# Optimization experiments

Hardware: AMD Instinct MI355X
Metric: run time of the kernel (lower is better)

Reference implementation:

```python
import jax, jax.numpy as jnp
import numpy as np

DT = 0.1
N_NODES = 100000
N_EDGES = 1600000
Q = 64


def setup_inputs() -> dict:
    key = jax.random.key(0)
    k1, k2, k3, k4, k5, k6, k7 = jax.random.split(key, 7)
    f = jax.random.uniform(k1, (N_NODES, Q), dtype=jnp.float32)
    collision = jax.random.normal(k2, (N_NODES, Q), dtype=jnp.float32)
    source = jax.random.normal(k3, (N_NODES, Q), dtype=jnp.float32)
    weight = jax.random.uniform(k4, (N_EDGES,), dtype=jnp.float32)
    xi = jax.random.normal(k5, (Q,), dtype=jnp.float32)
    src = jax.random.randint(k6, (N_EDGES,), 0, N_NODES)
    dst = jax.random.randint(k7, (N_EDGES,), 0, N_NODES)
    edge_index = jnp.stack([src, dst], axis=0)  # [2, E]
    return {
        "f_distribution": f,
        "collision_term": collision,
        "source_term": source,
        "edge_weight": weight,
        "xi_velocities": xi,
        "edge_index": edge_index,
    }


def reference(f_distribution, collision_term, source_term, edge_weight, xi_velocities, edge_index):
    src = edge_index[0]
    dst = edge_index[1]
    n = f_distribution.shape[0]

    # node degrees (DGL graph.out_degrees / in_degrees stored as ndata)
    ones_e = jnp.ones(src.shape[0], dtype=f_distribution.dtype)
    out_deg = jax.ops.segment_sum(ones_e, src, num_segments=n)
    in_deg = jax.ops.segment_sum(ones_e, dst, num_segments=n)
    out_deg = jnp.maximum(out_deg, 1.0)  # guard isolated nodes
    in_deg = jnp.maximum(in_deg, 1.0)

    f = jnp.clip(f_distribution, 0.0, None)

    # per-edge distribution difference f[dst] - f[src], shared by both passes
    f_diff = f[dst] - f[src]  # [E, Q]

    # inflow: message on original graph, q_ij = 1/out_degree(src), reduce at dst
    scale_in = (edge_weight / out_deg[src])[:, None] * xi_velocities[None, :]
    inflow = jax.ops.segment_sum(scale_in * f_diff, dst, num_segments=n)

    # outflow: on reversed graph: diff = f[rev_src]-f[rev_dst] = f[dst]-f[src],
    # q_ij = 1/in_degree(rev_dst) = 1/in_degree(src), reduce at rev_dst = src
    scale_out = (edge_weight / in_deg[src])[:, None] * xi_velocities[None, :]
    outflow = jax.ops.segment_sum(scale_out * f_diff, src, num_segments=n)

    transport = outflow - inflow
    f_new = f - DT * (transport - collision_term - source_term)
    return jnp.clip(f_new, 0.0, None)
```

## Files before the change

### kernel.cpp

```cpp
#include <hip/hip_runtime.h>

#define DT_CONST 0.1f
constexpr int Q = 64;
constexpr int SCAN_CHUNK = 1024;

constexpr int NPB = 128;
constexpr int CE  = 4096;
constexpr int EPC = 2 * CE;
constexpr int CAP = 4480;
constexpr int MAXCH = 512;
constexpr int P1T = 1024;

__global__ void count_kernel(const int* __restrict__ src, const int* __restrict__ dst,
                             int* __restrict__ cnt_out, int* __restrict__ cnt_in, int E) {
    int i = blockIdx.x * blockDim.x + threadIdx.x;
    int stride = gridDim.x * blockDim.x;
    for (int e = i; e < E; e += stride) {
        atomicAdd(&cnt_out[src[e]], 1);
        atomicAdd(&cnt_in[dst[e]], 1);
    }
}

__global__ __launch_bounds__(P1T, 8) void p1_kernel(
        const int* __restrict__ esrc, const int* __restrict__ edst,
        const float* __restrict__ w,
        const int* __restrict__ cnt_out, const int* __restrict__ cnt_in,
        int2* __restrict__ gstage, unsigned short* __restrict__ lofs_g,
        int E, int NB) {
    __shared__ int counts[1025];
    __shared__ int lofs[1025];
    __shared__ int work[1024];
    __shared__ alignas(16) int2 staged[EPC];

    int c = blockIdx.x;
    int e0 = c * CE;
    int ce = min(CE, E - e0);
    int tid = threadIdx.x;

    for (int i = tid; i < NB; i += P1T) counts[i] = 0;
    __syncthreads();

    int k4 = tid * 4;
    int4 se = make_int4(0, 0, 0, 0), de = make_int4(0, 0, 0, 0);
    float4 wv = make_float4(0.f, 0.f, 0.f, 0.f);
    int nmine = 0;
    if (k4 + 3 < ce) {
        se = *(const int4*)(esrc + e0 + k4);
        de = *(const int4*)(edst + e0 + k4);
        wv = *(const float4*)(w + e0 + k4);
        nmine = 4;
    } else if (k4 < ce) {
        int r = ce - k4;
        int* sp = &se.x; int* dp = &de.x; float* wp = &wv.x;
        for (int j = 0; j < r; ++j) {
            sp[j] = esrc[e0 + k4 + j];
            dp[j] = edst[e0 + k4 + j];
            wp[j] = w[e0 + k4 + j];
        }
        nmine = r;
    }
    {
        const int* sp = &se.x; const int* dp = &de.x;
        for (int j = 0; j < nmine; ++j) {
            atomicAdd(&counts[sp[j] >> 7], 1);
            atomicAdd(&counts[dp[j] >> 7], 1);
        }
    }
    __syncthreads();

    if (tid < 64) {
        int lane = tid;
        int carry = 0;
        for (int base = 0; base < NB; base += 64) {
            int idx = base + lane;
            int v = (idx < NB) ? counts[idx] : 0;
            int inc = v;
            for (int s = 1; s < 64; s <<= 1) {
                int t = __shfl_up(inc, s);
                if (lane >= s) inc += t;
            }
            if (idx < NB) lofs[idx] = carry + inc - v;
            carry += __shfl(inc, 63);
        }
        if (lane == 0) lofs[NB] = carry;
    }
    __syncthreads();

    for (int i = tid; i < NB; i += P1T) work[i] = lofs[i];
    __syncthreads();

    {
        const int* sp = &se.x; const int* dp = &de.x; const float* wp = &wv.x;
        for (int j = 0; j < nmine; ++j) {
            int s = sp[j], d = dp[j];
            float ww = wp[j];
            float w1 = ww / (float)max(cnt_in[s], 1);
            int pa = atomicAdd(&work[s >> 7], 1);
            staged[pa] = make_int2(((s & 127) << 17) | d, __float_as_int(w1));
            float w2 = ww / (float)max(cnt_out[s], 1);
            int pb = atomicAdd(&work[d >> 7], 1);
            staged[pb] = make_int2(((d & 127) << 17) | s, __float_as_int(w2));
        }
    }
    __syncthreads();

    int ne = 2 * ce;
    int4* gout4 = (int4*)(gstage + (size_t)c * EPC);
    const int4* st4 = (const int4*)staged;
    int ne2 = ne >> 1;
    for (int k = tid; k < ne2; k += P1T) gout4[k] = st4[k];
    if (ne & 1) { if (tid == 0) gstage[(size_t)c * EPC + ne - 1] = staged[ne - 1]; }
    unsigned short* lrow = lofs_g + (size_t)c * (NB + 1);
    for (int i = tid; i <= NB; i += P1T) lrow[i] = (unsigned short)lofs[i];
}

__global__ __launch_bounds__(512, 8) void pg_kernel(
        const float* __restrict__ f, const float* __restrict__ coll,
        const float* __restrict__ srct, const float* __restrict__ xi,
        const int* __restrict__ cnt_out, const int* __restrict__ cnt_in,
        const int2* __restrict__ gstage, const unsigned short* __restrict__ lofs_g,
        float* __restrict__ out, int N, int NB, int nchunks) {
    __shared__ unsigned short cum[MAXCH + 1];
    __shared__ unsigned short cstart[MAXCH];
    __shared__ int loff[NPB + 1];
    __shared__ int lcn[NPB];
    __shared__ int work[NPB];
    __shared__ alignas(16) int2 sorted[CAP];

    int b = blockIdx.x;
    int node0 = b * NPB;
    int nn = min(NPB, N - node0);
    int tid = threadIdx.x;
    int wid = tid >> 6, lane = tid & 63;

    for (int c = tid; c < nchunks; c += 512) {
        const unsigned short* lr = lofs_g + (size_t)c * (NB + 1);
        int lo = lr[b], hi = lr[b + 1];
        cstart[c] = (unsigned short)lo;
        cum[c] = (unsigned short)(hi - lo);
    }
    for (int i = tid; i < NPB; i += 512) {
        int v = node0 + i;
        lcn[i] = (i < nn) ? (cnt_out[v] + cnt_in[v]) : 0;
    }
    __syncthreads();

    if (wid == 0) {
        int carry = 0;
        for (int base = 0; base < nchunks; base += 64) {
            int idx = base + lane;
            int v = (idx < nchunks) ? (int)cum[idx] : 0;
            int inc = v;
            for (int s = 1; s < 64; s <<= 1) {
                int t = __shfl_up(inc, s);
                if (lane >= s) inc += t;
            }
            if (idx < nchunks) cum[idx] = (unsigned short)(carry + inc - v);
            carry += __shfl(inc, 63);
        }
        if (lane == 0) cum[nchunks] = (unsigned short)carry;
    }
    if (wid == 1) {
        int carry = 0;
        for (int base = 0; base < NPB; base += 64) {
            int idx = base + lane;
            int v = lcn[idx];
            int inc = v;
            for (int s = 1; s < 64; s <<= 1) {
                int t = __shfl_up(inc, s);
                if (lane >= s) inc += t;
            }
            loff[idx] = carry + inc - v;
            carry += __shfl(inc, 63);
        }
        if (lane == 0) loff[NPB] = carry;
    }
    __syncthreads();

    int tb = cum[nchunks];
    if (tb > CAP) tb = CAP;

    for (int i = tid; i < NPB; i += 512) work[i] = loff[i];
    __syncthreads();

    for (int r = tid; r < tb; r += 512) {
        int lo = 0, hi = nchunks - 1;
        while (lo < hi) {
            int mid = (lo + hi + 1) >> 1;
            if ((int)cum[mid] <= r) lo = mid; else hi = mid - 1;
        }
        int c = lo;
        int2 e = gstage[(size_t)c * EPC + (int)cstart[c] + (r - (int)cum[c])];
        int local = (e.x >> 17) & 127;
        int pos = atomicAdd(&work[local], 1);
        if (pos < CAP) sorted[pos] = make_int2(e.x & 131071, e.y);
    }
    __syncthreads();

    float xiv = xi[lane];
    for (int i = wid; i < nn; i += 8) {
        int st = loff[i], dg = lcn[i];
        float acc = 0.0f, S = 0.0f;
        int k = 0;
        for (; k + 8 <= dg; k += 8) {
            int2 e0 = sorted[st + k],     e1 = sorted[st + k + 1];
            int2 e2 = sorted[st + k + 2], e3 = sorted[st + k + 3];
            int2 e4 = sorted[st + k + 4], e5 = sorted[st + k + 5];
            int2 e6 = sorted[st + k + 6], e7 = sorted[st + k + 7];
            float f0 = f[(size_t)e0.x * Q + lane];
            float f1 = f[(size_t)e1.x * Q + lane];
            float f2 = f[(size_t)e2.x * Q + lane];
            float f3 = f[(size_t)e3.x * Q + lane];
            float f4 = f[(size_t)e4.x * Q + lane];
            float f5 = f[(size_t)e5.x * Q + lane];
            float f6 = f[(size_t)e6.x * Q + lane];
            float f7 = f[(size_t)e7.x * Q + lane];
            float w0 = __int_as_float(e0.y), w1 = __int_as_float(e1.y);
            float w2 = __int_as_float(e2.y), w3 = __int_as_float(e3.y);
            float w4 = __int_as_float(e4.y), w5 = __int_as_float(e5.y);
            float w6 = __int_as_float(e6.y), w7 = __int_as_float(e7.y);
            acc += w0 * fmaxf(f0, 0.0f); S += w0;
            acc += w1 * fmaxf(f1, 0.0f); S += w1;
            acc += w2 * fmaxf(f2, 0.0f); S += w2;
            acc += w3 * fmaxf(f3, 0.0f); S += w3;
            acc += w4 * fmaxf(f4, 0.0f); S += w4;
            acc += w5 * fmaxf(f5, 0.0f); S += w5;
            acc += w6 * fmaxf(f6, 0.0f); S += w6;
            acc += w7 * fmaxf(f7, 0.0f); S += w7;
        }
        for (; k < dg; ++k) {
            int2 e = sorted[st + k];
            float fn = f[(size_t)e.x * Q + lane];
            float wv = __int_as_float(e.y);
            acc += wv * fmaxf(fn, 0.0f); S += wv;
        }
        size_t idx = (size_t)(node0 + i) * Q + lane;
        float fv = fmaxf(f[idx], 0.0f);
        float t = xiv * (acc - fv * S);
        float r = fv - DT_CONST * (t - coll[idx] - srct[idx]);
        out[idx] = fmaxf(r, 0.0f);
    }
}

__global__ void scanA_kernel(const int* __restrict__ cnt_out, const int* __restrict__ cnt_in,
                             int* __restrict__ off_out, int* __restrict__ off_in,
                             int* __restrict__ bsum, int nblk, int n) {
    int b = blockIdx.x;
    const int* cnt; int* off; int* bs;
    if (b < nblk) { cnt = cnt_out; off = off_out; bs = bsum; }
    else          { cnt = cnt_in;  off = off_in;  bs = bsum + nblk; b -= nblk; }
    int i = b * SCAN_CHUNK + threadIdx.x;
    __shared__ int tmp[SCAN_CHUNK];
    int v = (i < n) ? cnt[i] : 0;
    tmp[threadIdx.x] = v;
    __syncthreads();
    for (int s = 1; s < SCAN_CHUNK; s <<= 1) {
        int t = (threadIdx.x >= (unsigned)s) ? tmp[threadIdx.x - s] : 0;
        __syncthreads();
        tmp[threadIdx.x] += t;
        __syncthreads();
    }
    if (i < n) off[i] = tmp[threadIdx.x] - v;
    if (threadIdx.x == SCAN_CHUNK - 1) bs[b] = tmp[SCAN_CHUNK - 1];
}

__global__ void scanB_kernel(int* __restrict__ bsum, int nblk) {
    __shared__ int tmp[SCAN_CHUNK];
    for (int dir = 0; dir < 2; ++dir) {
        int* bs = bsum + dir * nblk;
        int v = (threadIdx.x < (unsigned)nblk) ? bs[threadIdx.x] : 0;
        tmp[threadIdx.x] = v;
        __syncthreads();
        for (int s = 1; s < SCAN_CHUNK; s <<= 1) {
            int t = (threadIdx.x >= (unsigned)s) ? tmp[threadIdx.x - s] : 0;
            __syncthreads();
            tmp[threadIdx.x] += t;
            __syncthreads();
        }
        if (threadIdx.x < (unsigned)nblk) bs[threadIdx.x] = tmp[threadIdx.x] - v;
        __syncthreads();
    }
}

__global__ void scanC_kernel(int* __restrict__ off_out, int* __restrict__ off_in,
                             const int* __restrict__ bsum, int nblk, int n) {
    int b = blockIdx.x;
    bool isOut = b < nblk;
    int bb = isOut ? b : b - nblk;
    int i = bb * SCAN_CHUNK + threadIdx.x;
    if (i >= n) return;
    if (isOut) off_out[i] += bsum[b];
    else       off_in[i]  += bsum[b];
}

__global__ void fill_kernel(const int* __restrict__ src, const int* __restrict__ dst,
                            const float* __restrict__ w, const int* __restrict__ cnt_out,
                            int* __restrict__ off_out, int* __restrict__ off_in,
                            int2* __restrict__ pair_out, int2* __restrict__ pair_in, int E) {
    int i = blockIdx.x * blockDim.x + threadIdx.x;
    int stride = gridDim.x * blockDim.x;
    for (int e = i; e < E; e += stride) {
        int s = src[e], d = dst[e];
        float ww = w[e];
        int p = atomicAdd(&off_out[s], 1);
        pair_out[p] = make_int2(d, __float_as_int(ww));
        float sc = ww / (float)max(cnt_out[s], 1);
        int q = atomicAdd(&off_in[d], 1);
        pair_in[q] = make_int2(s, __float_as_int(sc));
    }
}

__global__ void gather_kernel(const float* __restrict__ f,
                              const float* __restrict__ coll,
                              const float* __restrict__ srct,
                              const float* __restrict__ xi,
                              const int* __restrict__ off_out, const int* __restrict__ cnt_out,
                              const int2* __restrict__ pair_out,
                              const int* __restrict__ off_in, const int* __restrict__ cnt_in,
                              const int2* __restrict__ pair_in,
                              float* __restrict__ out, int N) {
    int v = blockIdx.x * (blockDim.x >> 6) + (threadIdx.x >> 6);
    if (v >= N) return;
    int lane = threadIdx.x & 63;
    float fv = fmaxf(f[(size_t)v * Q + lane], 0.0f);
    float acc_out = 0.0f, acc_in = 0.0f;
    {
        int dg = cnt_out[v];
        int st = off_out[v] - dg;
        for (int base = 0; base < dg; base += 64) {
            int m = min(64, dg - base);
            int2 pr = make_int2(0, 0);
            if (lane < m) pr = pair_out[st + base + lane];
            for (int j = 0; j < m; ++j) {
                int   n2 = __shfl(pr.x, j);
                float w2 = __int_as_float(__shfl(pr.y, j));
                float fd = fmaxf(f[(size_t)n2 * Q + lane], 0.0f);
                acc_out += w2 * (fd - fv);
            }
        }
    }
    {
        int dg = cnt_in[v];
        int st = off_in[v] - dg;
        for (int base = 0; base < dg; base += 64) {
            int m = min(64, dg - base);
            int2 pr = make_int2(0, 0);
            if (lane < m) pr = pair_in[st + base + lane];
            for (int j = 0; j < m; ++j) {
                int   n2 = __shfl(pr.x, j);
                float w2 = __int_as_float(__shfl(pr.y, j));
                float fs = fmaxf(f[(size_t)n2 * Q + lane], 0.0f);
                acc_in += w2 * (fv - fs);
            }
        }
    }
    float indeg = (float)max(cnt_in[v], 1);
    float transport = xi[lane] * (acc_out / indeg - acc_in);
    size_t idx = (size_t)v * Q + lane;
    float r = fv - DT_CONST * (transport - coll[idx] - srct[idx]);
    out[idx] = fmaxf(r, 0.0f);
}

__global__ void deg_kernel(const int* __restrict__ src, const int* __restrict__ dst,
                           float* __restrict__ out_deg, float* __restrict__ in_deg, int E) {
    int i = blockIdx.x * blockDim.x + threadIdx.x;
    int stride = gridDim.x * blockDim.x;
    for (int e = i; e < E; e += stride) {
        atomicAdd(&out_deg[src[e]], 1.0f);
        atomicAdd(&in_deg[dst[e]], 1.0f);
    }
}

__global__ void scatter_kernel(const float* __restrict__ f, const float* __restrict__ w,
                               const float* __restrict__ xi, const int* __restrict__ src,
                               const int* __restrict__ dst, const float* __restrict__ out_deg,
                               const float* __restrict__ in_deg, float* __restrict__ transport,
                               int E) {
    int e = blockIdx.x * (blockDim.x >> 6) + (threadIdx.x >> 6);
    if (e >= E) return;
    int lane = threadIdx.x & 63;
    int s = src[e], d = dst[e];
    float ww = w[e];
    float s_out = ww / fmaxf(in_deg[s], 1.0f);
    float s_in  = ww / fmaxf(out_deg[s], 1.0f);
    float fs = fmaxf(f[(size_t)s * Q + lane], 0.0f);
    float fd = fmaxf(f[(size_t)d * Q + lane], 0.0f);
    float val = xi[lane] * (fd - fs);
    atomicAdd(&transport[(size_t)s * Q + lane],  s_out * val);
    atomicAdd(&transport[(size_t)d * Q + lane], -s_in  * val);
}

__global__ void final_kernel(const float* __restrict__ f, const float* __restrict__ coll,
                             const float* __restrict__ srct, float* __restrict__ out, int n4) {
    int i = blockIdx.x * blockDim.x + threadIdx.x;
    if (i >= n4) return;
    float4 t  = ((const float4*)out)[i];
    float4 fv = ((const float4*)f)[i];
    float4 c  = ((const float4*)coll)[i];
    float4 s  = ((const float4*)srct)[i];
    float4 r;
    r.x = fmaxf(fmaxf(fv.x, 0.0f) - DT_CONST * (t.x - c.x - s.x), 0.0f);
    r.y = fmaxf(fmaxf(fv.y, 0.0f) - DT_CONST * (t.y - c.y - s.y), 0.0f);
    r.z = fmaxf(fmaxf(fv.z, 0.0f) - DT_CONST * (t.z - c.z - s.z), 0.0f);
    r.w = fmaxf(fmaxf(fv.w, 0.0f) - DT_CONST * (t.w - c.w - s.w), 0.0f);
    ((float4*)out)[i] = r;
}

extern "C" void kernel_launch(void* const* d_in, const int* in_sizes, int n_in,
                              void* d_out, int out_size, void* d_ws, size_t ws_size,
                              hipStream_t stream) {
    const float* f    = (const float*)d_in[0];
    const float* coll = (const float*)d_in[1];
    const float* srct = (const float*)d_in[2];
    const float* w    = (const float*)d_in[3];
    const float* xi   = (const float*)d_in[4];
    const int*   eidx = (const int*)d_in[5];

    int N = in_sizes[0] / Q;
    int E = in_sizes[3];
    const int* esrc = eidx;
    const int* edst = eidx + E;
    float* out = (float*)d_out;

    int NB = (N + NPB - 1) / NPB;
    int nchunks = (E + CE - 1) / CE;
    size_t need1 = (size_t)nchunks * EPC * sizeof(int2)
                 + (size_t)2 * N * sizeof(int)
                 + (size_t)nchunks * (NB + 1) * sizeof(unsigned short);

    int nblk = (N + SCAN_CHUNK - 1) / SCAN_CHUNK;
    size_t need2 = ((size_t)4 * N + 2 * nblk + 256 + (size_t)4 * E) * 4;

    if (N <= 131072 && NB <= 1024 && nchunks <= MAXCH && ws_size >= need1) {
        int2* gstage = (int2*)d_ws;
        int* cnt_out = (int*)(gstage + (size_t)nchunks * EPC);
        int* cnt_in  = cnt_out + N;
        unsigned short* lofs = (unsigned short*)(cnt_in + N);

        hipMemsetAsync(cnt_out, 0, (size_t)2 * N * sizeof(int), stream);
        count_kernel<<<2048, 256, 0, stream>>>(esrc, edst, cnt_out, cnt_in, E);
        p1_kernel<<<nchunks, P1T, 0, stream>>>(esrc, edst, w, cnt_out, cnt_in,
                                               gstage, lofs, E, NB);
        pg_kernel<<<NB, 512, 0, stream>>>(f, coll, srct, xi,
                                          cnt_out, cnt_in, gstage, lofs,
                                          out, N, NB, nchunks);
    } else if (ws_size >= need2) {
        int* cnt_out = (int*)d_ws;
        int* cnt_in  = cnt_out + N;
        int* off_out = cnt_in + N;
        int* off_in  = off_out + N;
        int* bsum    = off_in + N;
        int2* pair_out = (int2*)(bsum + 2 * nblk + 256);
        int2* pair_in  = pair_out + E;

        hipMemsetAsync(cnt_out, 0, (size_t)2 * N * sizeof(int), stream);
        count_kernel<<<2048, 256, 0, stream>>>(esrc, edst, cnt_out, cnt_in, E);
        scanA_kernel<<<2 * nblk, SCAN_CHUNK, 0, stream>>>(cnt_out, cnt_in,
                                                          off_out, off_in, bsum, nblk, N);
        scanB_kernel<<<1, SCAN_CHUNK, 0, stream>>>(bsum, nblk);
        scanC_kernel<<<2 * nblk, SCAN_CHUNK, 0, stream>>>(off_out, off_in, bsum, nblk, N);
        fill_kernel<<<2048, 256, 0, stream>>>(esrc, edst, w, cnt_out,
                                              off_out, off_in, pair_out, pair_in, E);
        int gblocks = (N + 3) / 4;
        gather_kernel<<<gblocks, 256, 0, stream>>>(f, coll, srct, xi,
                                                   off_out, cnt_out, pair_out,
                                                   off_in, cnt_in, pair_in, out, N);
    } else {
        float* out_deg = (float*)d_ws;
        float* in_deg  = out_deg + N;
        hipMemsetAsync(out, 0, (size_t)N * Q * sizeof(float), stream);
        hipMemsetAsync(d_ws, 0, (size_t)2 * N * sizeof(float), stream);
        deg_kernel<<<1024, 256, 0, stream>>>(esrc, edst, out_deg, in_deg, E);
        int blocks = (E + 3) / 4;
        scatter_kernel<<<blocks, 256, 0, stream>>>(f, w, xi, esrc, edst,
                                                   out_deg, in_deg, out, E);
        int n4 = (N * Q) / 4;
        final_kernel<<<(n4 + 255) / 256, 256, 0, stream>>>(f, coll, srct, out, n4);
    }
}
```

Measured before the change: 406.6 us.

## Derive degrees from staged buckets, drop count kernel, gather neighbors in bf16

Removes the global-atomic count pass and the memset. p1 now stages raw weights plus a direction bit, and a new deg2 kernel derives packed in/out degrees per node block from the staged buckets. The gather kernel splits each node's edges into two bins: one normalised by the node's own in-degree, the other divided by the neighbour's out-degree, which is looked up per edge. p1 also converts clipped f to bf16 so the neighbour gathers read half the bytes. The cost is lower precision in the aggregated sums, an extra kernel that re-reads the staged edges, and extra random degree loads per outflow edge.

```diff
diff --git a/kernel.cpp b/kernel.cpp
--- a/kernel.cpp
+++ b/kernel.cpp
@@ -11,22 +11,20 @@
 constexpr int MAXCH = 512;
 constexpr int P1T = 1024;
 
-__global__ void count_kernel(const int* __restrict__ src, const int* __restrict__ dst,
-                             int* __restrict__ cnt_out, int* __restrict__ cnt_in, int E) {
-    int i = blockIdx.x * blockDim.x + threadIdx.x;
-    int stride = gridDim.x * blockDim.x;
-    for (int e = i; e < E; e += stride) {
-        atomicAdd(&cnt_out[src[e]], 1);
-        atomicAdd(&cnt_in[dst[e]], 1);
-    }
-}
-
+__device__ inline unsigned short f2bf_clip(float x) {
+    x = fmaxf(x, 0.0f);
+    unsigned u = __float_as_uint(x);
+    u += 0x7FFF + ((u >> 16) & 1);
+    return (unsigned short)(u >> 16);
+}
+
+template<bool CVT>
 __global__ __launch_bounds__(P1T, 8) void p1_kernel(
         const int* __restrict__ esrc, const int* __restrict__ edst,
-        const float* __restrict__ w,
-        const int* __restrict__ cnt_out, const int* __restrict__ cnt_in,
+        const float* __restrict__ w, const float* __restrict__ f,
+        unsigned short* __restrict__ fb,
         int2* __restrict__ gstage, unsigned short* __restrict__ lofs_g,
-        int E, int NB) {
+        int E, int NB, int N) {
     __shared__ int counts[1025];
     __shared__ int lofs[1025];
     __shared__ int work[1024];
@@ -36,6 +34,18 @@
     int e0 = c * CE;
     int ce = min(CE, E - e0);
     int tid = threadIdx.x;
+
+    if (CVT) {
+        size_t n4 = (size_t)N * Q / 4;
+        size_t gthreads = (size_t)gridDim.x * P1T;
+        for (size_t i = (size_t)c * P1T + tid; i < n4; i += gthreads) {
+            float4 v = ((const float4*)f)[i];
+            ushort4 o;
+            o.x = f2bf_clip(v.x); o.y = f2bf_clip(v.y);
+            o.z = f2bf_clip(v.z); o.w = f2bf_clip(v.w);
+            ((ushort4*)fb)[i] = o;
+        }
+    }
 
     for (int i = tid; i < NB; i += P1T) counts[i] = 0;
     __syncthreads();
@@ -93,13 +103,11 @@
         const int* sp = &se.x; const int* dp = &de.x; const float* wp = &wv.x;
         for (int j = 0; j < nmine; ++j) {
             int s = sp[j], d = dp[j];
-            float ww = wp[j];
-            float w1 = ww / (float)max(cnt_in[s], 1);
+            int wb = __float_as_int(wp[j]);
             int pa = atomicAdd(&work[s >> 7], 1);
-            staged[pa] = make_int2(((s & 127) << 17) | d, __float_as_int(w1));
-            float w2 = ww / (float)max(cnt_out[s], 1);
+            staged[pa] = make_int2(((s & 127) << 17) | d, wb);
             int pb = atomicAdd(&work[d >> 7], 1);
-            staged[pb] = make_int2(((d & 127) << 17) | s, __float_as_int(w2));
+            staged[pb] = make_int2(0x1000000 | ((d & 127) << 17) | s, wb);
         }
     }
     __syncthreads();
@@ -109,40 +117,31 @@
     const int4* st4 = (const int4*)staged;
     int ne2 = ne >> 1;
     for (int k = tid; k < ne2; k += P1T) gout4[k] = st4[k];
-    if (ne & 1) { if (tid == 0) gstage[(size_t)c * EPC + ne - 1] = staged[ne - 1]; }
+    if ((ne & 1) && tid == 0) gstage[(size_t)c * EPC + ne - 1] = staged[ne - 1];
     unsigned short* lrow = lofs_g + (size_t)c * (NB + 1);
     for (int i = tid; i <= NB; i += P1T) lrow[i] = (unsigned short)lofs[i];
 }
 
-__global__ __launch_bounds__(512, 8) void pg_kernel(
-        const float* __restrict__ f, const float* __restrict__ coll,
-        const float* __restrict__ srct, const float* __restrict__ xi,
-        const int* __restrict__ cnt_out, const int* __restrict__ cnt_in,
+__global__ __launch_bounds__(256) void deg2_kernel(
         const int2* __restrict__ gstage, const unsigned short* __restrict__ lofs_g,
-        float* __restrict__ out, int N, int NB, int nchunks) {
+        int* __restrict__ deg, int N, int NB, int nchunks) {
     __shared__ unsigned short cum[MAXCH + 1];
     __shared__ unsigned short cstart[MAXCH];
-    __shared__ int loff[NPB + 1];
-    __shared__ int lcn[NPB];
-    __shared__ int work[NPB];
-    __shared__ alignas(16) int2 sorted[CAP];
+    __shared__ int cnt[NPB];
 
     int b = blockIdx.x;
     int node0 = b * NPB;
     int nn = min(NPB, N - node0);
     int tid = threadIdx.x;
-    int wid = tid >> 6, lane = tid & 63;
-
-    for (int c = tid; c < nchunks; c += 512) {
+    int lane = tid & 63, wid = tid >> 6;
+
+    for (int c = tid; c < nchunks; c += 256) {
         const unsigned short* lr = lofs_g + (size_t)c * (NB + 1);
         int lo = lr[b], hi = lr[b + 1];
         cstart[c] = (unsigned short)lo;
         cum[c] = (unsigned short)(hi - lo);
     }
-    for (int i = tid; i < NPB; i += 512) {
-        int v = node0 + i;
-        lcn[i] = (i < nn) ? (cnt_out[v] + cnt_in[v]) : 0;
-    }
+    for (int i = tid; i < NPB; i += 256) cnt[i] = 0;
     __syncthreads();
 
     if (wid == 0) {
@@ -160,11 +159,76 @@
         }
         if (lane == 0) cum[nchunks] = (unsigned short)carry;
     }
+    __syncthreads();
+
+    int tb = cum[nchunks];
+    for (int r = tid; r < tb; r += 256) {
+        int lo = 0, hi = nchunks - 1;
+        while (lo < hi) {
+            int mid = (lo + hi + 1) >> 1;
+            if ((int)cum[mid] <= r) lo = mid; else hi = mid - 1;
+        }
+        int c = lo;
+        int x = gstage[(size_t)c * EPC + (int)cstart[c] + (r - (int)cum[c])].x;
+        int local = (x >> 17) & 127;
+        int t = (x >> 24) & 1;
+        atomicAdd(&cnt[local], 1 << (t * 16));
+    }
+    __syncthreads();
+    for (int i = tid; i < nn; i += 256) deg[node0 + i] = cnt[i];
+}
+
+template<bool BF16>
+__global__ __launch_bounds__(512, 8) void pg_kernel(
+        const float* __restrict__ f, const unsigned short* __restrict__ fb,
+        const float* __restrict__ coll, const float* __restrict__ srct,
+        const float* __restrict__ xi, const int* __restrict__ deg_g,
+        const int2* __restrict__ gstage, const unsigned short* __restrict__ lofs_g,
+        float* __restrict__ out, int N, int NB, int nchunks) {
+    __shared__ unsigned short cum[MAXCH + 1];
+    __shared__ unsigned short cstart[MAXCH];
+    __shared__ int loff[2 * NPB + 1];
+    __shared__ int work[2 * NPB];
+    __shared__ int degl[NPB];
+    __shared__ alignas(16) int2 sorted[CAP];
+
+    int b = blockIdx.x;
+    int node0 = b * NPB;
+    int nn = min(NPB, N - node0);
+    int tid = threadIdx.x;
+    int wid = tid >> 6, lane = tid & 63;
+
+    for (int c = tid; c < nchunks; c += 512) {
+        const unsigned short* lr = lofs_g + (size_t)c * (NB + 1);
+        int lo = lr[b], hi = lr[b + 1];
+        cstart[c] = (unsigned short)lo;
+        cum[c] = (unsigned short)(hi - lo);
+    }
+    for (int i = tid; i < NPB; i += 512)
+        degl[i] = (i < nn) ? deg_g[node0 + i] : 0;
+    __syncthreads();
+
+    if (wid == 0) {
+        int carry = 0;
+        for (int base = 0; base < nchunks; base += 64) {
+            int idx = base + lane;
+            int v = (idx < nchunks) ? (int)cum[idx] : 0;
+            int inc = v;
+            for (int s = 1; s < 64; s <<= 1) {
+                int t = __shfl_up(inc, s);
+                if (lane >= s) inc += t;
+            }
+            if (idx < nchunks) cum[idx] = (unsigned short)(carry + inc - v);
+            carry += __shfl(inc, 63);
+        }
+        if (lane == 0) cum[nchunks] = (unsigned short)carry;
+    }
     if (wid == 1) {
         int carry = 0;
-        for (int base = 0; base < NPB; base += 64) {
+        for (int base = 0; base < 2 * NPB; base += 64) {
             int idx = base + lane;
-            int v = lcn[idx];
+            int d = degl[idx >> 1];
+            int v = (idx & 1) ? (d >> 16) : (d & 0xFFFF);
             int inc = v;
             for (int s = 1; s < 64; s <<= 1) {
                 int t = __shfl_up(inc, s);
@@ -173,14 +237,14 @@
             loff[idx] = carry + inc - v;
             carry += __shfl(inc, 63);
         }
-        if (lane == 0) loff[NPB] = carry;
+        if (lane == 0) loff[2 * NPB] = carry;
     }
     __syncthreads();
 
     int tb = cum[nchunks];
     if (tb > CAP) tb = CAP;
 
-    for (int i = tid; i < NPB; i += 512) work[i] = loff[i];
+    for (int i = tid; i < 2 * NPB; i += 512) work[i] = loff[i];
     __syncthreads();
 
     for (int r = tid; r < tb; r += 512) {
@@ -192,53 +256,84 @@
         int c = lo;
         int2 e = gstage[(size_t)c * EPC + (int)cstart[c] + (r - (int)cum[c])];
         int local = (e.x >> 17) & 127;
-        int pos = atomicAdd(&work[local], 1);
-        if (pos < CAP) sorted[pos] = make_int2(e.x & 131071, e.y);
+        int bin = local * 2 + ((e.x >> 24) & 1);
+        int pos = atomicAdd(&work[bin], 1);
+        if (pos < CAP) sorted[pos] = make_int2(e.x & 0x1FFFF, e.y);
     }
     __syncthreads();
 
     float xiv = xi[lane];
     for (int i = wid; i < nn; i += 8) {
-        int st = loff[i], dg = lcn[i];
-        float acc = 0.0f, S = 0.0f;
-        int k = 0;
-        for (; k + 8 <= dg; k += 8) {
-            int2 e0 = sorted[st + k],     e1 = sorted[st + k + 1];
-            int2 e2 = sorted[st + k + 2], e3 = sorted[st + k + 3];
-            int2 e4 = sorted[st + k + 4], e5 = sorted[st + k + 5];
-            int2 e6 = sorted[st + k + 6], e7 = sorted[st + k + 7];
-            float f0 = f[(size_t)e0.x * Q + lane];
-            float f1 = f[(size_t)e1.x * Q + lane];
-            float f2 = f[(size_t)e2.x * Q + lane];
-            float f3 = f[(size_t)e3.x * Q + lane];
-            float f4 = f[(size_t)e4.x * Q + lane];
-            float f5 = f[(size_t)e5.x * Q + lane];
-            float f6 = f[(size_t)e6.x * Q + lane];
-            float f7 = f[(size_t)e7.x * Q + lane];
+        int dl = degl[i];
+        float rin = __fdividef(1.0f, (float)max(dl >> 16, 1));
+        int stA = min(loff[2 * i], CAP);
+        int mid = min(loff[2 * i + 1], CAP);
+        int end = min(loff[2 * i + 2], CAP);
+        float accA = 0.0f, SA = 0.0f, accB = 0.0f, SB = 0.0f;
+
+#define LOADF(nbr) (BF16 ? __uint_as_float((unsigned)fb[(size_t)(nbr) * Q + lane] << 16) \
+                         : fmaxf(f[(size_t)(nbr) * Q + lane], 0.0f))
+        int k = stA;
+        for (; k + 8 <= mid; k += 8) {
+            int2 e0 = sorted[k],     e1 = sorted[k + 1];
+            int2 e2 = sorted[k + 2], e3 = sorted[k + 3];
+            int2 e4 = sorted[k + 4], e5 = sorted[k + 5];
+            int2 e6 = sorted[k + 6], e7 = sorted[k + 7];
+            float f0 = LOADF(e0.x), f1 = LOADF(e1.x), f2 = LOADF(e2.x), f3 = LOADF(e3.x);
+            float f4 = LOADF(e4.x), f5 = LOADF(e5.x), f6 = LOADF(e6.x), f7 = LOADF(e7.x);
             float w0 = __int_as_float(e0.y), w1 = __int_as_float(e1.y);
             float w2 = __int_as_float(e2.y), w3 = __int_as_float(e3.y);
             float w4 = __int_as_float(e4.y), w5 = __int_as_float(e5.y);
             float w6 = __int_as_float(e6.y), w7 = __int_as_float(e7.y);
-            acc += w0 * fmaxf(f0, 0.0f); S += w0;
-            acc += w1 * fmaxf(f1, 0.0f); S += w1;
-            acc += w2 * fmaxf(f2, 0.0f); S += w2;
-            acc += w3 * fmaxf(f3, 0.0f); S += w3;
-            acc += w4 * fmaxf(f4, 0.0f); S += w4;
-            acc += w5 * fmaxf(f5, 0.0f); S += w5;
-            acc += w6 * fmaxf(f6, 0.0f); S += w6;
-            acc += w7 * fmaxf(f7, 0.0f); S += w7;
-        }
-        for (; k < dg; ++k) {
-            int2 e = sorted[st + k];
-            float fn = f[(size_t)e.x * Q + lane];
+            accA += w0 * f0; SA += w0;  accA += w1 * f1; SA += w1;
+            accA += w2 * f2; SA += w2;  accA += w3 * f3; SA += w3;
+            accA += w4 * f4; SA += w4;  accA += w5 * f5; SA += w5;
+            accA += w6 * f6; SA += w6;  accA += w7 * f7; SA += w7;
+        }
+        for (; k < mid; ++k) {
+            int2 e = sorted[k];
+            float fn = LOADF(e.x);
             float wv = __int_as_float(e.y);
-            acc += wv * fmaxf(fn, 0.0f); S += wv;
-        }
+            accA += wv * fn; SA += wv;
+        }
+        for (k = mid; k + 4 <= end; k += 4) {
+            int2 e0 = sorted[k],     e1 = sorted[k + 1];
+            int2 e2 = sorted[k + 2], e3 = sorted[k + 3];
+            int d0 = deg_g[e0.x] & 0xFFFF, d1 = deg_g[e1.x] & 0xFFFF;
+            int d2 = deg_g[e2.x] & 0xFFFF, d3 = deg_g[e3.x] & 0xFFFF;
+            float f0 = LOADF(e0.x), f1 = LOADF(e1.x), f2 = LOADF(e2.x), f3 = LOADF(e3.x);
+            float s0 = __fdividef(__int_as_float(e0.y), (float)max(d0, 1));
+            float s1 = __fdividef(__int_as_float(e1.y), (float)max(d1, 1));
+            float s2 = __fdividef(__int_as_float(e2.y), (float)max(d2, 1));
+            float s3 = __fdividef(__int_as_float(e3.y), (float)max(d3, 1));
+            accB += s0 * f0; SB += s0;  accB += s1 * f1; SB += s1;
+            accB += s2 * f2; SB += s2;  accB += s3 * f3; SB += s3;
+        }
+        for (; k < end; ++k) {
+            int2 e = sorted[k];
+            int dv = deg_g[e.x] & 0xFFFF;
+            float fn = LOADF(e.x);
+            float sc = __fdividef(__int_as_float(e.y), (float)max(dv, 1));
+            accB += sc * fn; SB += sc;
+        }
+#undef LOADF
+        float acc = accA * rin + accB;
+        float S   = SA * rin + SB;
         size_t idx = (size_t)(node0 + i) * Q + lane;
         float fv = fmaxf(f[idx], 0.0f);
         float t = xiv * (acc - fv * S);
         float r = fv - DT_CONST * (t - coll[idx] - srct[idx]);
         out[idx] = fmaxf(r, 0.0f);
+    }
+}
+
+__global__ void count_kernel(const int* __restrict__ src, const int* __restrict__ dst,
+                             int* __restrict__ cnt_out, int* __restrict__ cnt_in, int E) {
+    int i = blockIdx.x * blockDim.x + threadIdx.x;
+    int stride = gridDim.x * blockDim.x;
+    for (int e = i; e < E; e += stride) {
+        atomicAdd(&cnt_out[src[e]], 1);
+        atomicAdd(&cnt_in[dst[e]], 1);
     }
 }
 
@@ -424,26 +519,39 @@
 
     int NB = (N + NPB - 1) / NPB;
     int nchunks = (E + CE - 1) / CE;
-    size_t need1 = (size_t)nchunks * EPC * sizeof(int2)
-                 + (size_t)2 * N * sizeof(int)
-                 + (size_t)nchunks * (NB + 1) * sizeof(unsigned short);
+
+    size_t gbytes  = (size_t)nchunks * EPC * sizeof(int2);
+    size_t fbbytes = (size_t)N * Q * sizeof(unsigned short);
+    size_t degbyts = (size_t)N * sizeof(int);
+    size_t lbytes  = (size_t)nchunks * (NB + 1) * sizeof(unsigned short);
+    size_t need_f32 = gbytes + degbyts + lbytes;
+    size_t need_b16 = gbytes + fbbytes + degbyts + lbytes;
 
     int nblk = (N + SCAN_CHUNK - 1) / SCAN_CHUNK;
     size_t need2 = ((size_t)4 * N + 2 * nblk + 256 + (size_t)4 * E) * 4;
 
-    if (N <= 131072 && NB <= 1024 && nchunks <= MAXCH && ws_size >= need1) {
-        int2* gstage = (int2*)d_ws;
-        int* cnt_out = (int*)(gstage + (size_t)nchunks * EPC);
-        int* cnt_in  = cnt_out + N;
-        unsigned short* lofs = (unsigned short*)(cnt_in + N);
-
-        hipMemsetAsync(cnt_out, 0, (size_t)2 * N * sizeof(int), stream);
-        count_kernel<<<2048, 256, 0, stream>>>(esrc, edst, cnt_out, cnt_in, E);
-        p1_kernel<<<nchunks, P1T, 0, stream>>>(esrc, edst, w, cnt_out, cnt_in,
-                                               gstage, lofs, E, NB);
-        pg_kernel<<<NB, 512, 0, stream>>>(f, coll, srct, xi,
-                                          cnt_out, cnt_in, gstage, lofs,
-                                          out, N, NB, nchunks);
+    if (N <= 131072 && NB <= 1024 && nchunks <= MAXCH && ws_size >= need_f32) {
+        bool use_bf16 = (ws_size >= need_b16);
+        char* p = (char*)d_ws;
+        int2* gstage = (int2*)p;            p += gbytes;
+        unsigned short* fb = nullptr;
+        if (use_bf16) { fb = (unsigned short*)p; p += fbbytes; }
+        int* deg = (int*)p;                 p += degbyts;
+        unsigned short* lofs = (unsigned short*)p;
+
+        if (use_bf16)
+            p1_kernel<true><<<nchunks, P1T, 0, stream>>>(esrc, edst, w, f, fb,
+                                                         gstage, lofs, E, NB, N);
+        else
+            p1_kernel<false><<<nchunks, P1T, 0, stream>>>(esrc, edst, w, f, fb,
+                                                          gstage, lofs, E, NB, N);
+        deg2_kernel<<<NB, 256, 0, stream>>>(gstage, lofs, deg, N, NB, nchunks);
+        if (use_bf16)
+            pg_kernel<true><<<NB, 512, 0, stream>>>(f, fb, coll, srct, xi, deg,
+                                                    gstage, lofs, out, N, NB, nchunks);
+        else
+            pg_kernel<false><<<NB, 512, 0, stream>>>(f, fb, coll, srct, xi, deg,
+                                                     gstage, lofs, out, N, NB, nchunks);
     } else if (ws_size >= need2) {
         int* cnt_out = (int*)d_ws;
         int* cnt_in  = cnt_out + N;
```

New measurement: 331.0 us. 18.6% less time.
